# Optimization experiments

Measured on AMD Instinct MI355X. Metric: run time of the kernel, lower is better.

The kernel has to match this reference:

```python
import jax, jax.numpy as jnp
import numpy as np

B, S_IMG, S_TXT, H, D = 1, 2048, 512, 24, 128
HID = H * D  # 3072
S_TOT = S_TXT + S_IMG
IP_SCALE = 1.0
EPS = 1e-5


def setup_inputs() -> dict:
    key = jax.random.key(0)
    ks = jax.random.split(key, 16)
    r = lambda k, s: jax.random.normal(k, s, dtype=jnp.float32)
    w = lambda k, s: r(k, s) * 0.02
    theta = r(ks[15], (S_TOT, D))  # rotary angles over joint sequence
    z = lambda: jnp.zeros((HID,), jnp.float32)
    return dict(
        hidden_states=r(ks[0], (B, S_IMG, HID)),
        encoder_hidden_states=r(ks[1], (B, S_TXT, HID)),
        image_emb=r(ks[2], (B, 4, HID)),
        rope_cos=jnp.cos(theta), rope_sin=jnp.sin(theta),
        Wq=w(ks[3], (HID, HID)), bq=z(),
        Wk=w(ks[4], (HID, HID)), bk=z(),
        Wv=w(ks[5], (HID, HID)), bv=z(),
        Waq=w(ks[6], (HID, HID)), baq=z(),
        Wak=w(ks[7], (HID, HID)), bak=z(),
        Wav=w(ks[8], (HID, HID)), bav=z(),
        Wk_ip=w(ks[9], (HID, HID)),
        Wv_ip=w(ks[10], (HID, HID)),
        Wo=w(ks[11], (HID, HID)), bo=z(),
        Wao=w(ks[12], (HID, HID)), bao=z(),
    )


def _heads(x):  # [B,S,HID] -> [B,H,S,D]
    return x.reshape(x.shape[0], x.shape[1], H, D).transpose(0, 2, 1, 3)


def _unheads(x):  # [B,H,S,D] -> [B,S,HID]
    return x.transpose(0, 2, 1, 3).reshape(x.shape[0], x.shape[2], HID)


def _rmsnorm(x):  # over last dim, no affine (RMSNorm(128, affine=False))
    return x * jax.lax.rsqrt(jnp.mean(x * x, axis=-1, keepdims=True) + EPS)


def _rope(x, cos, sin):  # diffusers apply_rotary_emb, use_real, interleaved pairs
    xp = x.reshape(*x.shape[:-1], D // 2, 2)
    rot = jnp.stack([-xp[..., 1], xp[..., 0]], axis=-1).reshape(x.shape)
    return x * cos + rot * sin  # cos/sin [S,D] broadcast over [B,H,S,D]


def _sdpa(q, k, v):
    s = jnp.einsum('bhqd,bhkd->bhqk', q, k) / jnp.sqrt(jnp.asarray(D, q.dtype))
    return jnp.einsum('bhqk,bhkd->bhqd', jax.nn.softmax(s, axis=-1), v)


def _forward(hidden_states, encoder_hidden_states, image_emb, rope_cos, rope_sin,
             Wq, bq, Wk, bk, Wv, bv, Waq, baq, Wak, bak, Wav, bav,
             Wk_ip, Wv_ip, Wo, bo, Wao, bao):
    # main QKV over image-latent tokens
    q = _rmsnorm(_heads(hidden_states @ Wq.T + bq))
    k = _rmsnorm(_heads(hidden_states @ Wk.T + bk))
    v = _heads(hidden_states @ Wv.T + bv)
    # IP-adapter cross attention (query = latent q, kv from image_emb)
    k_ip = _rmsnorm(_heads(image_emb @ Wk_ip.T))
    v_ip = _heads(image_emb @ Wv_ip.T)
    ip_out = _unheads(_sdpa(q, k_ip, v_ip))  # [B,S_IMG,HID]
    # encoder (text) QKV, concat text-first as in Flux
    eq = _rmsnorm(_heads(encoder_hidden_states @ Waq.T + baq))
    ek = _rmsnorm(_heads(encoder_hidden_states @ Wak.T + bak))
    ev = _heads(encoder_hidden_states @ Wav.T + bav)
    q = jnp.concatenate([eq, q], axis=2)
    k = jnp.concatenate([ek, k], axis=2)
    v = jnp.concatenate([ev, v], axis=2)
    q = _rope(q, rope_cos, rope_sin)
    k = _rope(k, rope_cos, rope_sin)
    out = _unheads(_sdpa(q, k, v))  # [B,S_TOT,HID]
    enc_out, hid_out = out[:, :S_TXT], out[:, S_TXT:]
    hid_out = hid_out + IP_SCALE * ip_out
    hid_out = hid_out @ Wo.T + bo   # to_out[0] (+ identity dropout)
    enc_out = enc_out @ Wao.T + bao  # to_add_out
    return hid_out, enc_out


def reference(hidden_states, encoder_hidden_states, image_emb, rope_cos, rope_sin,
              Wq, bq, Wk, bk, Wv, bv, Waq, baq, Wak, bak, Wav, bav,
              Wk_ip, Wv_ip, Wo, bo, Wao, bao):
    return _forward(hidden_states, encoder_hidden_states, image_emb, rope_cos, rope_sin,
                    Wq, bq, Wk, bk, Wv, bv, Waq, baq, Wak, bak, Wav, bav,
                    Wk_ip, Wv_ip, Wo, bo, Wao, bao)
```

## Files before the change

### kernel.cpp

```cpp
#include <hip/hip_runtime.h>

typedef __bf16 bf16;
typedef __bf16 bf16x2 __attribute__((ext_vector_type(2)));
typedef __bf16 bf16x4 __attribute__((ext_vector_type(4)));
typedef __bf16 bf16x8 __attribute__((ext_vector_type(8)));
typedef float  f32x4  __attribute__((ext_vector_type(4)));

#define H_    24
#define D_    128
#define HID_  3072
#define SIMG_ 2048
#define STXT_ 512
#define STOT_ 2560
#define EPS_  1e-5f
#define SCALE_ 0.08838834764831845f
#define HH_   ((size_t)HID_*HID_)

typedef __attribute__((address_space(3))) unsigned int lds_uint;
typedef const __attribute__((address_space(1))) unsigned int glb_uint;
__device__ __forceinline__ void gll16(const void* g, void* l){
  __builtin_amdgcn_global_load_lds((glb_uint*)g, (lds_uint*)l, 16, 0, 0);
}

__device__ inline bf16x8 frag8f(const float* __restrict__ p){
  const f32x4 a = *(const f32x4*)p;
  const f32x4 b = *(const f32x4*)(p + 4);
  bf16x8 r;
  r[0]=(bf16)a[0]; r[1]=(bf16)a[1]; r[2]=(bf16)a[2]; r[3]=(bf16)a[3];
  r[4]=(bf16)b[0]; r[5]=(bf16)b[1]; r[6]=(bf16)b[2]; r[7]=(bf16)b[3];
  return r;
}

__device__ __forceinline__ void cvt8(const float* __restrict__ s, bf16* __restrict__ d, int i){
  const f32x4 a = *(const f32x4*)(s + i);
  const f32x4 b = *(const f32x4*)(s + i + 4);
  bf16x8 o;
  o[0]=(bf16)a[0]; o[1]=(bf16)a[1]; o[2]=(bf16)a[2]; o[3]=(bf16)a[3];
  o[4]=(bf16)b[0]; o[5]=(bf16)b[1]; o[6]=(bf16)b[2]; o[7]=(bf16)b[3];
  *(bf16x8*)(d + i) = o;
}

#define CONV_BLK 2048
__global__ __launch_bounds__(256) void k_prep(
    const float* __restrict__ HS, const float* __restrict__ ENC,
    const float* __restrict__ W0, const float* __restrict__ W1,
    const float* __restrict__ W2, const float* __restrict__ W3,
    const float* __restrict__ W4, const float* __restrict__ W5,
    const float* __restrict__ W6, const float* __restrict__ W7,
    const float* __restrict__ IMG,
    const float* __restrict__ Wkip, const float* __restrict__ Wvip,
    bf16* __restrict__ HSb, bf16* __restrict__ ENCb, bf16* __restrict__ Wb8,
    float* __restrict__ Kip, float* __restrict__ Vip)
{
  __shared__ float tile[4][128];
  const int bx = (int)blockIdx.x;
  const int t = (int)threadIdx.x;
  if (bx < 48){
    const bool isV = (bx >= 24);
    const int h = bx % 24;
    const float* Wm = isV ? Wvip : Wkip;
    const int w = t >> 6, l = t & 63;
    const int lr = l & 15, lg = l >> 4;
    const int col0 = h*128 + w*32;
    f32x4 acc0 = {}, acc1 = {};
    const float* arow = IMG + (size_t)((lr < 4) ? lr : 0)*HID_;
    const float* wr0 = Wm + (size_t)(col0 + lr)*HID_;
    const float* wr1 = Wm + (size_t)(col0 + 16 + lr)*HID_;
    for (int k0 = 0; k0 < HID_; k0 += 32){
      const bf16x8 af = frag8f(arow + k0 + lg*8);
      acc0 = __builtin_amdgcn_mfma_f32_16x16x32_bf16(af, frag8f(wr0 + k0 + lg*8), acc0, 0, 0, 0);
      acc1 = __builtin_amdgcn_mfma_f32_16x16x32_bf16(af, frag8f(wr1 + k0 + lg*8), acc1, 0, 0, 0);
    }
    if (lg == 0){
      #pragma unroll
      for (int r = 0; r < 4; r++){
        tile[r][w*32 + lr]      = acc0[r];
        tile[r][w*32 + 16 + lr] = acc1[r];
      }
    }
    __syncthreads();
    if (isV){
      const int e = t*2;
      const int j = e >> 7, d = e & 127;
      Vip[(size_t)(h*4 + j)*D_ + d]     = tile[j][d];
      Vip[(size_t)(h*4 + j)*D_ + d + 1] = tile[j][d + 1];
    } else {
      const float v0 = tile[w][2*l], v1 = tile[w][2*l + 1];
      float ss = v0*v0 + v1*v1;
      #pragma unroll
      for (int m = 1; m < 64; m <<= 1) ss += __shfl_xor(ss, m);
      const float rk = rsqrtf(ss*(1.0f/128.0f) + EPS_);
      Kip[(size_t)(h*4 + w)*D_ + 2*l]     = v0*rk;
      Kip[(size_t)(h*4 + w)*D_ + 2*l + 1] = v1*rk;
    }
  } else {
    for (int c = bx - 48; c < 20352; c += CONV_BLK){
      const float* s; bf16* d; int base;
      if (c < 1536){ s = HS;  d = HSb;  base = c*4096; }
      else if (c < 1920){ s = ENC; d = ENCb; base = (c - 1536)*4096; }
      else {
        const int idx = c - 1920;
        const int wi = idx / 2304;
        s = (wi==0)?W0:(wi==1)?W1:(wi==2)?W2:(wi==3)?W3:(wi==4)?W4:(wi==5)?W5:(wi==6)?W6:W7;
        d = Wb8 + (size_t)wi*HH_;
        base = (idx % 2304)*4096;
      }
      const int i = base + t*16;
      cvt8(s, d, i);
      cvt8(s, d, i + 8);
    }
  }
}

#define MFMA_ __builtin_amdgcn_mfma_f32_16x16x32_bf16
#define MM(bfr, n) \
    acc[0][n]=MFMA_(af0,bfr,acc[0][n],0,0,0); acc[1][n]=MFMA_(af1,bfr,acc[1][n],0,0,0); \
    acc[2][n]=MFMA_(af2,bfr,acc[2][n],0,0,0); acc[3][n]=MFMA_(af3,bfr,acc[3][n],0,0,0);
#define WAIT6  asm volatile("s_waitcnt vmcnt(6)" ::: "memory")
#define WAIT0  asm volatile("s_waitcnt vmcnt(0)" ::: "memory")
#define NOWAIT (void)0

__device__ __forceinline__ void gemm8_core(
    const bf16* __restrict__ A, const bf16* __restrict__ W,
    int mb, int nb,
    f32x4 (&acc)[4][4],
    bf16 (&Al)[3][128][64],
    bf16 (&Bl)[3][256][64])
{
  const int t = (int)threadIdx.x;
  const int w = t >> 6, l = t & 63;
  const int lr = l & 15, lg = l >> 4;
  const int wr = w >> 2, wc = w & 3;
  const int srow = t >> 3;
  const int soff = ((t & 7) ^ (srow & 7)) * 8;

  const bf16* Abase = A + (size_t)(mb + srow)*HID_ + soff;
  const bf16* Wbase = W + (size_t)(nb + srow)*HID_ + soff;

#define SA(buf, tt, i) gll16(Abase + (size_t)(i)*64*HID_ + (tt)*64, &Al[buf][0][0] + (i)*4096 + t*8)
#define SB(buf, tt, i) gll16(Wbase + (size_t)(i)*64*HID_ + (tt)*64, &Bl[buf][0][0] + (i)*4096 + t*8)

  const int arow_ = wr*64 + lr;
  const int brow_ = wc*64 + lr;
  const int sx = lr & 7;

  SA(0,0,0); SA(0,0,1); SB(0,0,0); SB(0,0,1); SB(0,0,2); SB(0,0,3);
  SA(1,1,0); SA(1,1,1); SB(1,1,0); SB(1,1,1); SB(1,1,2); SB(1,1,3);
  WAIT6;
  __builtin_amdgcn_s_barrier();

#define TILE(C, NXT, TT, PRE, TW)                                            \
  {                                                                          \
    const int s0_ = (lg^sx)*8, s1_ = ((4+lg)^sx)*8;                          \
    bf16x8 af0,af1,af2,af3,b0,b1;                                            \
    af0=*(const bf16x8*)&Al[C][arow_   ][s0_];                               \
    af1=*(const bf16x8*)&Al[C][arow_+16][s0_];                               \
    af2=*(const bf16x8*)&Al[C][arow_+32][s0_];                               \
    af3=*(const bf16x8*)&Al[C][arow_+48][s0_];                               \
    b0 =*(const bf16x8*)&Bl[C][brow_   ][s0_];                               \
    b1 =*(const bf16x8*)&Bl[C][brow_+16][s0_];                               \
    if (PRE){ SA(NXT,(TT)+2,0); SA(NXT,(TT)+2,1); }                          \
    __builtin_amdgcn_s_setprio(1); MM(b0,0) MM(b1,1)                         \
    __builtin_amdgcn_s_setprio(0);                                           \
    b0 =*(const bf16x8*)&Bl[C][brow_+32][s0_];                               \
    b1 =*(const bf16x8*)&Bl[C][brow_+48][s0_];                               \
    if (PRE){ SB(NXT,(TT)+2,0); SB(NXT,(TT)+2,1); }                          \
    __builtin_amdgcn_s_setprio(1); MM(b0,2) MM(b1,3)                         \
    __builtin_amdgcn_s_setprio(0);                                           \
    af0=*(const bf16x8*)&Al[C][arow_   ][s1_];                               \
    af1=*(const bf16x8*)&Al[C][arow_+16][s1_];                               \
    af2=*(const bf16x8*)&Al[C][arow_+32][s1_];                               \
    af3=*(const bf16x8*)&Al[C][arow_+48][s1_];                               \
    b0 =*(const bf16x8*)&Bl[C][brow_   ][s1_];                               \
    b1 =*(const bf16x8*)&Bl[C][brow_+16][s1_];                               \
    if (PRE){ SB(NXT,(TT)+2,2); SB(NXT,(TT)+2,3); }                          \
    __builtin_amdgcn_s_setprio(1); MM(b0,0) MM(b1,1)                         \
    __builtin_amdgcn_s_setprio(0);                                           \
    b0 =*(const bf16x8*)&Bl[C][brow_+32][s1_];                               \
    b1 =*(const bf16x8*)&Bl[C][brow_+48][s1_];                               \
    __builtin_amdgcn_s_setprio(1); MM(b0,2) MM(b1,3)                         \
    __builtin_amdgcn_s_setprio(0);                                           \
    TW;                                                                      \
    __builtin_amdgcn_s_barrier();                                            \
  }

  for (int base = 0; base < 45; base += 3){
    TILE(0, 2, base,   true, WAIT6);
    TILE(1, 0, base+1, true, WAIT6);
    TILE(2, 1, base+2, true, WAIT6);
  }
  TILE(0, 2, 45, true,  WAIT6);
  TILE(1, 0, 46, false, WAIT0);
  TILE(2, 1, 47, false, NOWAIT);
#undef TILE
#undef SA
#undef SB
}

__global__ __launch_bounds__(512, 1) void k_gemm8_qkv(
    const bf16* __restrict__ Ahid, const bf16* __restrict__ Aenc,
    const bf16* __restrict__ Wb,
    const float* bq, const float* bk, const float* bv,
    const float* baq, const float* bak, const float* bav,
    bf16* Cq, bf16* Ck, bf16* Cv, bf16* Ceq, bf16* Cek, bf16* Cev)
{
  __shared__ __align__(16) bf16 Al[3][128][64];
  __shared__ __align__(16) bf16 Bl[3][256][64];
  const int lin = (int)blockIdx.x;
  const int work = (lin & 7)*90 + (lin >> 3);
  const int mt = work / 36;
  const int ct = work % 36;
  const int which = ct % 3;
  const int nb = (ct/3)*256;
  const int enc = (mt >= 16) ? 1 : 0;
  const int mb = (enc ? (mt - 16) : mt)*128;
  const bf16* A = enc ? Aenc : Ahid;
  const int widx = which + enc*3;
  const bf16* W = Wb + (size_t)widx*HH_;
  const float* bias = (which==0) ? (enc?baq:bq) : (which==1) ? (enc?bak:bk) : (enc?bav:bv);
  bf16* Cm = (which==0) ? (enc?Ceq:Cq) : (which==1) ? (enc?Cek:Ck) : (enc?Cev:Cv);

  f32x4 acc[4][4] = {};
  gemm8_core(A, W, mb, nb, acc, Al, Bl);

  const int w = (int)(threadIdx.x >> 6), l = (int)(threadIdx.x & 63u);
  const int lr = l & 15, lg = l >> 4;
  const int wr = w >> 2, wc = w & 3;
  #pragma unroll
  for (int nf = 0; nf < 4; nf++){
    const int col = nb + wc*64 + nf*16 + lr;
    const float bvl = bias[col];
    #pragma unroll
    for (int m = 0; m < 4; m++){
      #pragma unroll
      for (int r = 0; r < 4; r++){
        const int row = mb + wr*64 + m*16 + lg*4 + r;
        Cm[(size_t)row*HID_ + col] = (bf16)(acc[m][nf][r] + bvl);
      }
    }
  }
}

__global__ __launch_bounds__(512, 1) void k_gemm8_out(
    const bf16* __restrict__ Ahid, const bf16* __restrict__ Aenc,
    const bf16* __restrict__ Wb,
    const float* bo, const float* bao, float* __restrict__ outp)
{
  __shared__ __align__(16) bf16 Al[3][128][64];
  __shared__ __align__(16) bf16 Bl[3][256][64];
  const int lin = (int)blockIdx.x;
  const int work = (lin & 7)*30 + (lin >> 3);
  const int mt = work / 12;
  const int nb = (work % 12)*256;
  const int enc = (mt >= 16) ? 1 : 0;
  const int mb = (enc ? (mt - 16) : mt)*128;
  const bf16* A = enc ? Aenc : Ahid;
  const bf16* W = Wb + (size_t)(enc ? 7 : 6)*HH_;
  const float* bias = enc ? bao : bo;
  float* C = outp + (enc ? (size_t)SIMG_*HID_ : 0);

  f32x4 acc[4][4] = {};
  gemm8_core(A, W, mb, nb, acc, Al, Bl);

  const int w = (int)(threadIdx.x >> 6), l = (int)(threadIdx.x & 63u);
  const int lr = l & 15, lg = l >> 4;
  const int wr = w >> 2, wc = w & 3;
  #pragma unroll
  for (int nf = 0; nf < 4; nf++){
    const int col = nb + wc*64 + nf*16 + lr;
    const float bvl = bias[col];
    #pragma unroll
    for (int m = 0; m < 4; m++){
      #pragma unroll
      for (int r = 0; r < 4; r++){
        const int row = mb + wr*64 + m*16 + lg*4 + r;
        C[(size_t)row*HID_ + col] = acc[m][nf][r] + bvl;
      }
    }
  }
}

__global__ __launch_bounds__(256) void k_finish_qk2(
    const bf16* __restrict__ rawQ, const bf16* __restrict__ rawK,
    const bf16* __restrict__ rawEQ, const bf16* __restrict__ rawEK,
    const float* __restrict__ cosT, const float* __restrict__ sinT,
    const float* __restrict__ Kip, const float* __restrict__ Vip,
    bf16* __restrict__ Qh, bf16* __restrict__ Kh, bf16* __restrict__ ipOut)
{
  const int wid = (int)blockIdx.x*4 + (int)(threadIdx.x >> 6);
  const int l = (int)(threadIdx.x & 63u);
  const int s = wid / H_;
  const int h = wid % H_;
  const bf16 *sq_, *sk_;
  if (s < STXT_){
    const size_t off = (size_t)s*HID_ + h*D_;
    sq_ = rawEQ + off; sk_ = rawEK + off;
  } else {
    const size_t off = (size_t)(s - STXT_)*HID_ + h*D_;
    sq_ = rawQ + off; sk_ = rawK + off;
  }
  const int d0 = 2*l, d1 = 2*l + 1;
  float q0 = sq_[d0], q1 = sq_[d1];
  float k0 = sk_[d0], k1 = sk_[d1];
  float ssq = q0*q0 + q1*q1;
  float ssk = k0*k0 + k1*k1;
  #pragma unroll
  for (int m = 1; m < 64; m <<= 1){ ssq += __shfl_xor(ssq, m); ssk += __shfl_xor(ssk, m); }
  const float rq = rsqrtf(ssq*(1.0f/128.0f) + EPS_);
  const float rk = rsqrtf(ssk*(1.0f/128.0f) + EPS_);
  q0 *= rq; q1 *= rq; k0 *= rk; k1 *= rk;
  const float c0 = cosT[(size_t)s*D_ + d0], c1 = cosT[(size_t)s*D_ + d1];
  const float s0 = sinT[(size_t)s*D_ + d0], s1 = sinT[(size_t)s*D_ + d1];
  const float qo0 = q0*c0 - q1*s0, qo1 = q1*c1 + q0*s1;
  const float ko0 = k0*c0 - k1*s0, ko1 = k1*c1 + k0*s1;
  const size_t qoff = ((size_t)h*STOT_ + s)*D_ + d0;
  Qh[qoff] = (bf16)qo0; Qh[qoff + 1] = (bf16)qo1;
  Kh[qoff] = (bf16)ko0; Kh[qoff + 1] = (bf16)ko1;

  if (s >= STXT_){
    const float* kb = Kip + (size_t)h*4*D_;
    const float* vb = Vip + (size_t)h*4*D_;
    float sc[4];
    #pragma unroll
    for (int j = 0; j < 4; j++) sc[j] = q0*kb[j*D_ + d0] + q1*kb[j*D_ + d1];
    #pragma unroll
    for (int m = 1; m < 64; m <<= 1){
      #pragma unroll
      for (int j = 0; j < 4; j++) sc[j] += __shfl_xor(sc[j], m);
    }
    const float mx = fmaxf(fmaxf(sc[0], sc[1]), fmaxf(sc[2], sc[3]));
    float p[4], ps = 0.f;
    #pragma unroll
    for (int j = 0; j < 4; j++){ p[j] = __expf((sc[j] - mx)*SCALE_); ps += p[j]; }
    const float inv = 1.0f/ps;
    float o0 = 0.f, o1 = 0.f;
    #pragma unroll
    for (int j = 0; j < 4; j++){ o0 += p[j]*vb[j*D_ + d0]; o1 += p[j]*vb[j*D_ + d1]; }
    const size_t dst = (size_t)(s - STXT_)*HID_ + h*D_;
    ipOut[dst + d0] = (bf16)(o0*inv);
    ipOut[dst + d1] = (bf16)(o1*inv);
  }
}

__global__ __launch_bounds__(256) void k_vtrans(
    const bf16* __restrict__ rawV, const bf16* __restrict__ rawEV,
    bf16* __restrict__ Vt)
{
  __shared__ bf16 lt[128*130];
  const int t = (int)threadIdx.x;
  const int stile = (int)blockIdx.x*128;
  const int h = (int)blockIdx.y;
  #pragma unroll
  for (int i = 0; i < 8; i++){
    const int sl = i*16 + (t >> 4);
    const int s = stile + sl;
    const bf16* src = (s < STXT_) ? (rawEV + (size_t)s*HID_) : (rawV + (size_t)(s - STXT_)*HID_);
    const bf16x8 v = *(const bf16x8*)(src + h*D_ + (t & 15)*8);
    #pragma unroll
    for (int j = 0; j < 8; j++) lt[((t & 15)*8 + j)*130 + sl] = v[j];
  }
  __syncthreads();
  #pragma unroll
  for (int j = 0; j < 4; j++){
    const int d = j*32 + (t >> 3);
    const int s0 = (t & 7)*16;
    bf16x8 a, b;
    #pragma unroll
    for (int k = 0; k < 4; k++){
      const bf16x2 p = *(const bf16x2*)(lt + d*130 + s0 + 2*k);
      a[2*k] = p[0]; a[2*k+1] = p[1];
    }
    #pragma unroll
    for (int k = 0; k < 4; k++){
      const bf16x2 p = *(const bf16x2*)(lt + d*130 + s0 + 8 + 2*k);
      b[2*k] = p[0]; b[2*k+1] = p[1];
    }
    bf16* dst = Vt + ((size_t)h*D_ + d)*STOT_ + stile + s0;
    *(bf16x8*)dst = a;
    *(bf16x8*)(dst + 8) = b;
  }
}

__global__ __launch_bounds__(256, 2) void k_flash3(
    const bf16* __restrict__ Q, const bf16* __restrict__ K,
    const bf16* __restrict__ Vt, const bf16* __restrict__ ipOut,
    bf16* __restrict__ attnOut)
{
  __shared__ __align__(16) bf16 Ks[2][64*128];
  __shared__ __align__(16) bf16 Vs[2][128*64];
  __shared__ __align__(16) bf16 plds[4][32*64];
  const int t = (int)threadIdx.x;
  const int w = t >> 6, l = t & 63;
  const int lr = l & 15, lg = l >> 4;
  const int lin = (int)blockIdx.x;
  const int work = (lin & 7)*60 + (lin >> 3);
  const int h = work / 20;
  const int qbase = (work % 20)*128 + w*32;
  const bf16* Qh = Q  + (size_t)h*STOT_*D_;
  const bf16* Kh = K  + (size_t)h*STOT_*D_;
  const bf16* Vh = Vt + (size_t)h*D_*STOT_;

  bf16x8 qf[2][4];
  #pragma unroll
  for (int qt = 0; qt < 2; qt++)
    #pragma unroll
    for (int kk = 0; kk < 4; kk++)
      qf[qt][kk] = *(const bf16x8*)(Qh + (size_t)(qbase + qt*16 + lr)*D_ + kk*32 + lg*8);

  f32x4 acc[2][8] = {};
  float mrun[2] = {-3.0e38f, -3.0e38f}, lrun[2] = {0.f, 0.f};

  const int krow = t >> 4, kslot = t & 15;
  const int vrow = t >> 3, vslot = t & 7;

  auto STAGE = [&](int buf, int kv){
    #pragma unroll
    for (int i = 0; i < 4; i++){
      const int r = i*16 + krow;
      gll16(Kh + (size_t)(kv + r)*D_ + ((kslot ^ (r & 7))*8),
            (void*)(&Ks[buf][0] + (size_t)t*8 + i*2048));
    }
    #pragma unroll
    for (int i = 0; i < 4; i++){
      const int r = i*32 + vrow;
      gll16(Vh + (size_t)r*STOT_ + kv + ((vslot ^ (r & 7))*8),
            (void*)(&Vs[buf][0] + (size_t)t*8 + i*2048));
    }
  };

  STAGE(0, 0);
  __syncthreads();
  int cur = 0;
  for (int kv = 0; kv < STOT_; kv += 64){
    if (kv + 64 < STOT_) STAGE(cur ^ 1, kv + 64);

    f32x4 st[2][4] = {};
    #pragma unroll
    for (int tt = 0; tt < 4; tt++){
      const int kr = tt*16 + lr;
      #pragma unroll
      for (int kk = 0; kk < 4; kk++){
        const bf16x8 kf = *(const bf16x8*)(&Ks[cur][0] + kr*128 + (((kk*4 + lg) ^ (kr & 7))*8));
        st[0][tt] = __builtin_amdgcn_mfma_f32_16x16x32_bf16(kf, qf[0][kk], st[0][tt], 0, 0, 0);
        st[1][tt] = __builtin_amdgcn_mfma_f32_16x16x32_bf16(kf, qf[1][kk], st[1][tt], 0, 0, 0);
      }
    }
    #pragma unroll
    for (int qt = 0; qt < 2; qt++){
      const int q = qt*16 + lr;
      float sv[4][4];
      float vmax = -3.0e38f;
      #pragma unroll
      for (int tt = 0; tt < 4; tt++)
        #pragma unroll
        for (int r = 0; r < 4; r++){ const float x = st[qt][tt][r]*SCALE_; sv[tt][r] = x; vmax = fmaxf(vmax, x); }
      vmax = fmaxf(vmax, __shfl_xor(vmax, 16));
      vmax = fmaxf(vmax, __shfl_xor(vmax, 32));
      const float mnew  = fmaxf(mrun[qt], vmax);
      const float alpha = __expf(mrun[qt] - mnew);
      float rs = 0.f;
      #pragma unroll
      for (int tt = 0; tt < 4; tt++){
        bf16x4 pq;
        #pragma unroll
        for (int r = 0; r < 4; r++){
          const float p = __expf(sv[tt][r] - mnew);
          rs += p;
          pq[r] = (bf16)p;
        }
        *(bf16x4*)(&plds[w][q*64 + (((tt*2 + (lg >> 1)) ^ (q & 7))*8) + (lg & 1)*4]) = pq;
      }
      rs += __shfl_xor(rs, 16);
      rs += __shfl_xor(rs, 32);
      lrun[qt] = lrun[qt]*alpha + rs;
      mrun[qt] = mnew;
      #pragma unroll
      for (int n = 0; n < 8; n++)
        #pragma unroll
        for (int r = 0; r < 4; r++) acc[qt][n][r] *= alpha;
    }
    #pragma unroll
    for (int ks = 0; ks < 2; ks++){
      const bf16x8 pb0 = *(const bf16x8*)(&plds[w][(lr)*64      + (((ks*4 + lg) ^ (lr & 7))*8)]);
      const bf16x8 pb1 = *(const bf16x8*)(&plds[w][(16 + lr)*64 + (((ks*4 + lg) ^ (lr & 7))*8)]);
      #pragma unroll
      for (int n = 0; n < 8; n++){
        const int vr = n*16 + lr;
        const bf16x8 vf = *(const bf16x8*)(&Vs[cur][0] + vr*64 + (((ks*4 + lg) ^ (vr & 7))*8));
        acc[0][n] = __builtin_amdgcn_mfma_f32_16x16x32_bf16(vf, pb0, acc[0][n], 0, 0, 0);
        acc[1][n] = __builtin_amdgcn_mfma_f32_16x16x32_bf16(vf, pb1, acc[1][n], 0, 0, 0);
      }
    }
    __syncthreads();
    cur ^= 1;
  }
  const bool hid = (qbase >= STXT_);
  #pragma unroll
  for (int qt = 0; qt < 2; qt++){
    const float inv = 1.0f/lrun[qt];
    const int row = qbase + qt*16 + lr;
    #pragma unroll
    for (int n = 0; n < 8; n++){
      const size_t cbase = (size_t)row*HID_ + h*D_ + n*16 + lg*4;
      if (hid){
        const bf16x4 ip = *(const bf16x4*)(ipOut + (size_t)(row - STXT_)*HID_ + h*D_ + n*16 + lg*4);
        bf16x4 o;
        #pragma unroll
        for (int r = 0; r < 4; r++) o[r] = (bf16)(acc[qt][n][r]*inv + (float)ip[r]);
        *(bf16x4*)(attnOut + cbase) = o;
      } else {
        bf16x4 o;
        #pragma unroll
        for (int r = 0; r < 4; r++) o[r] = (bf16)(acc[qt][n][r]*inv);
        *(bf16x4*)(attnOut + cbase) = o;
      }
    }
  }
}

extern "C" void kernel_launch(void* const* d_in, const int* in_sizes, int n_in,
                              void* d_out, int out_size, void* d_ws, size_t ws_size,
                              hipStream_t stream)
{
  const float* HS   = (const float*)d_in[0];
  const float* ENC  = (const float*)d_in[1];
  const float* IMG  = (const float*)d_in[2];
  const float* COS  = (const float*)d_in[3];
  const float* SIN  = (const float*)d_in[4];
  const float* Wq   = (const float*)d_in[5];  const float* bq  = (const float*)d_in[6];
  const float* Wk   = (const float*)d_in[7];  const float* bk  = (const float*)d_in[8];
  const float* Wv   = (const float*)d_in[9];  const float* bv  = (const float*)d_in[10];
  const float* Waq  = (const float*)d_in[11]; const float* baq = (const float*)d_in[12];
  const float* Wak  = (const float*)d_in[13]; const float* bak = (const float*)d_in[14];
  const float* Wav  = (const float*)d_in[15]; const float* bav = (const float*)d_in[16];
  const float* Wkip = (const float*)d_in[17]; const float* Wvip= (const float*)d_in[18];
  const float* Wo   = (const float*)d_in[19]; const float* bo  = (const float*)d_in[20];
  const float* Wao  = (const float*)d_in[21]; const float* bao = (const float*)d_in[22];

  char* wsb = (char*)d_ws;
  size_t off = 0;
  auto alloc = [&](size_t bytes) -> char* {
    char* p = wsb + off; off += (bytes + 255) & ~((size_t)255); return p;
  };
  bf16* rawQ   = (bf16*)alloc((size_t)SIMG_*HID_*2);
  bf16* rawK   = (bf16*)alloc((size_t)SIMG_*HID_*2);
  bf16* rawV   = (bf16*)alloc((size_t)SIMG_*HID_*2);
  bf16* rawEQ  = (bf16*)alloc((size_t)STXT_*HID_*2);
  bf16* rawEK  = (bf16*)alloc((size_t)STXT_*HID_*2);
  bf16* rawEV  = (bf16*)alloc((size_t)STXT_*HID_*2);
  bf16* Qb     = (bf16*)alloc((size_t)H_*STOT_*D_*2);
  bf16* Kb     = (bf16*)alloc((size_t)H_*STOT_*D_*2);
  bf16* Vtb    = (bf16*)alloc((size_t)H_*STOT_*D_*2);
  bf16* AOUT   = (bf16*)alloc((size_t)STOT_*HID_*2);
  bf16* IPOUT  = (bf16*)alloc((size_t)SIMG_*HID_*2);
  float* KIPF  = (float*)alloc((size_t)H_*4*D_*4);
  float* VIPF  = (float*)alloc((size_t)H_*4*D_*4);
  bf16* HSb    = (bf16*)alloc((size_t)SIMG_*HID_*2);
  bf16* ENCb   = (bf16*)alloc((size_t)STXT_*HID_*2);
  bf16* Wb8    = (bf16*)alloc((size_t)8*HH_*2);

  dim3 blk(256);
  dim3 blk512(512);
  k_prep<<<dim3(48 + CONV_BLK), blk, 0, stream>>>(HS, ENC, Wq, Wk, Wv, Waq, Wak, Wav, Wo, Wao,
                                                  IMG, Wkip, Wvip, HSb, ENCb, Wb8, KIPF, VIPF);
  k_gemm8_qkv<<<dim3(720), blk512, 0, stream>>>(HSb, ENCb, Wb8,
                                                bq, bk, bv, baq, bak, bav,
                                                rawQ, rawK, rawV, rawEQ, rawEK, rawEV);
  k_finish_qk2<<<dim3(15360), blk, 0, stream>>>(rawQ, rawK, rawEQ, rawEK, COS, SIN,
                                                KIPF, VIPF, Qb, Kb, IPOUT);
  k_vtrans<<<dim3(20,24), blk, 0, stream>>>(rawV, rawEV, Vtb);
  k_flash3<<<dim3(480), blk, 0, stream>>>(Qb, Kb, Vtb, IPOUT, AOUT);
  float* outp = (float*)d_out;
  k_gemm8_out<<<dim3(240), blk512, 0, stream>>>(AOUT + (size_t)STXT_*HID_, AOUT, Wb8, bo, bao, outp);
}
```

Baseline: 547.1 us.

## Restructure GEMM core to 4-wave blocks with 32-wide K tiles and two blocks per CU

Replaces the 8-wave 128x256 GEMM core (64-wide K slices, 48 iterations) with a 4-wave version that keeps the same 128x256 output tile but gives each wave a 64x128 sub-tile (32 accumulators). K is streamed in 32-wide slices over 96 iterations, using a new swizzled LDS layout that packs two rows per 64-element line. LDS per block halves, so launch bounds allow two blocks per CU, aiming for better latency hiding and fewer LDS reads per MFMA. In exchange, register pressure per wave doubles and barriers are twice as frequent.

```diff
diff --git a/kernel.cpp b/kernel.cpp
--- a/kernel.cpp
+++ b/kernel.cpp
@@ -113,99 +113,113 @@
 }
 
 #define MFMA_ __builtin_amdgcn_mfma_f32_16x16x32_bf16
-#define MM(bfr, n) \
-    acc[0][n]=MFMA_(af0,bfr,acc[0][n],0,0,0); acc[1][n]=MFMA_(af1,bfr,acc[1][n],0,0,0); \
-    acc[2][n]=MFMA_(af2,bfr,acc[2][n],0,0,0); acc[3][n]=MFMA_(af3,bfr,acc[3][n],0,0,0);
 #define WAIT6  asm volatile("s_waitcnt vmcnt(6)" ::: "memory")
 #define WAIT0  asm volatile("s_waitcnt vmcnt(0)" ::: "memory")
 #define NOWAIT (void)0
 
-__device__ __forceinline__ void gemm8_core(
+__device__ __forceinline__ void gemm4_core(
     const bf16* __restrict__ A, const bf16* __restrict__ W,
     int mb, int nb,
-    f32x4 (&acc)[4][4],
-    bf16 (&Al)[3][128][64],
-    bf16 (&Bl)[3][256][64])
+    f32x4 (&acc)[4][8],
+    bf16 (&Al)[3][4096],
+    bf16 (&Bl)[3][8192])
 {
   const int t = (int)threadIdx.x;
   const int w = t >> 6, l = t & 63;
   const int lr = l & 15, lg = l >> 4;
-  const int wr = w >> 2, wc = w & 3;
-  const int srow = t >> 3;
-  const int soff = ((t & 7) ^ (srow & 7)) * 8;
-
-  const bf16* Abase = A + (size_t)(mb + srow)*HID_ + soff;
-  const bf16* Wbase = W + (size_t)(nb + srow)*HID_ + soff;
-
-#define SA(buf, tt, i) gll16(Abase + (size_t)(i)*64*HID_ + (tt)*64, &Al[buf][0][0] + (i)*4096 + t*8)
-#define SB(buf, tt, i) gll16(Wbase + (size_t)(i)*64*HID_ + (tt)*64, &Bl[buf][0][0] + (i)*4096 + t*8)
-
-  const int arow_ = wr*64 + lr;
-  const int brow_ = wc*64 + lr;
-  const int sx = lr & 7;
-
-  SA(0,0,0); SA(0,0,1); SB(0,0,0); SB(0,0,1); SB(0,0,2); SB(0,0,3);
-  SA(1,1,0); SA(1,1,1); SB(1,1,0); SB(1,1,1); SB(1,1,2); SB(1,1,3);
-  WAIT6;
-  __builtin_amdgcn_s_barrier();
-
-#define TILE(C, NXT, TT, PRE, TW)                                            \
+  const int wr = w >> 1, wc = w & 1;
+
+  const int gdA0 = t,        gdA1 = 256 + t;
+  const int lA0 = gdA0 >> 3, lA1 = gdA1 >> 3;
+  const int gA0 = (gdA0 & 7) ^ (lA0 & 7), gA1 = (gdA1 & 7) ^ (lA1 & 7);
+  const bf16* Asrc0 = A + (size_t)(mb + 2*lA0 + (gA0 >> 2))*HID_ + (gA0 & 3)*8;
+  const bf16* Asrc1 = A + (size_t)(mb + 2*lA1 + (gA1 >> 2))*HID_ + (gA1 & 3)*8;
+  const int dA0 = gdA0*8, dA1 = gdA1*8;
+
+  const bf16* Bsrc0; const bf16* Bsrc1; const bf16* Bsrc2; const bf16* Bsrc3;
+  int dB0, dB1, dB2, dB3;
+  {
+    const int g0 = t, g1 = 256 + t, g2 = 512 + t, g3 = 768 + t;
+    const int l0 = g0>>3, l1 = g1>>3, l2 = g2>>3, l3 = g3>>3;
+    const int u0 = (g0&7)^(l0&7), u1 = (g1&7)^(l1&7), u2 = (g2&7)^(l2&7), u3 = (g3&7)^(l3&7);
+    Bsrc0 = W + (size_t)(nb + 2*l0 + (u0>>2))*HID_ + (u0&3)*8;
+    Bsrc1 = W + (size_t)(nb + 2*l1 + (u1>>2))*HID_ + (u1&3)*8;
+    Bsrc2 = W + (size_t)(nb + 2*l2 + (u2>>2))*HID_ + (u2&3)*8;
+    Bsrc3 = W + (size_t)(nb + 2*l3 + (u3>>2))*HID_ + (u3&3)*8;
+    dB0 = g0*8; dB1 = g1*8; dB2 = g2*8; dB3 = g3*8;
+  }
+
+#define SA4(buf, TT)  { gll16(Asrc0 + (TT)*32, &Al[buf][0] + dA0); \
+                        gll16(Asrc1 + (TT)*32, &Al[buf][0] + dA1); }
+#define SB4a(buf, TT) { gll16(Bsrc0 + (TT)*32, &Bl[buf][0] + dB0); \
+                        gll16(Bsrc1 + (TT)*32, &Bl[buf][0] + dB1); }
+#define SB4b(buf, TT) { gll16(Bsrc2 + (TT)*32, &Bl[buf][0] + dB2); \
+                        gll16(Bsrc3 + (TT)*32, &Bl[buf][0] + dB3); }
+
+  const int gx = ((((lr & 1) << 2) | lg) ^ ((lr >> 1) & 7)) * 8;
+  const int baseA = (wr*32 + (lr >> 1))*64 + gx;
+  const int baseB = (wc*64 + (lr >> 1))*64 + gx;
+
+#define MMN(bb, n) \
+    acc[0][n]=MFMA_(a0,bb,acc[0][n],0,0,0); acc[1][n]=MFMA_(a1,bb,acc[1][n],0,0,0); \
+    acc[2][n]=MFMA_(a2,bb,acc[2][n],0,0,0); acc[3][n]=MFMA_(a3,bb,acc[3][n],0,0,0);
+
+#define TILE4(C, NXT, TT, PRE, TW)                                           \
   {                                                                          \
-    const int s0_ = (lg^sx)*8, s1_ = ((4+lg)^sx)*8;                          \
-    bf16x8 af0,af1,af2,af3,b0,b1;                                            \
-    af0=*(const bf16x8*)&Al[C][arow_   ][s0_];                               \
-    af1=*(const bf16x8*)&Al[C][arow_+16][s0_];                               \
-    af2=*(const bf16x8*)&Al[C][arow_+32][s0_];                               \
-    af3=*(const bf16x8*)&Al[C][arow_+48][s0_];                               \
-    b0 =*(const bf16x8*)&Bl[C][brow_   ][s0_];                               \
-    b1 =*(const bf16x8*)&Bl[C][brow_+16][s0_];                               \
-    if (PRE){ SA(NXT,(TT)+2,0); SA(NXT,(TT)+2,1); }                          \
-    __builtin_amdgcn_s_setprio(1); MM(b0,0) MM(b1,1)                         \
+    bf16x8 a0,a1,a2,a3,b0,b1,b2,b3;                                          \
+    a0 = *(const bf16x8*)(&Al[C][0] + baseA);                                \
+    a1 = *(const bf16x8*)(&Al[C][0] + baseA + 512);                          \
+    a2 = *(const bf16x8*)(&Al[C][0] + baseA + 1024);                         \
+    a3 = *(const bf16x8*)(&Al[C][0] + baseA + 1536);                         \
+    b0 = *(const bf16x8*)(&Bl[C][0] + baseB);                                \
+    b1 = *(const bf16x8*)(&Bl[C][0] + baseB + 512);                          \
+    b2 = *(const bf16x8*)(&Bl[C][0] + baseB + 1024);                         \
+    b3 = *(const bf16x8*)(&Bl[C][0] + baseB + 1536);                         \
+    if (PRE){ SA4(NXT, (TT)+2); SB4a(NXT, (TT)+2); }                         \
+    __builtin_amdgcn_s_setprio(1);                                           \
+    MMN(b0,0) MMN(b1,1) MMN(b2,2) MMN(b3,3)                                  \
     __builtin_amdgcn_s_setprio(0);                                           \
-    b0 =*(const bf16x8*)&Bl[C][brow_+32][s0_];                               \
-    b1 =*(const bf16x8*)&Bl[C][brow_+48][s0_];                               \
-    if (PRE){ SB(NXT,(TT)+2,0); SB(NXT,(TT)+2,1); }                          \
-    __builtin_amdgcn_s_setprio(1); MM(b0,2) MM(b1,3)                         \
-    __builtin_amdgcn_s_setprio(0);                                           \
-    af0=*(const bf16x8*)&Al[C][arow_   ][s1_];                               \
-    af1=*(const bf16x8*)&Al[C][arow_+16][s1_];                               \
-    af2=*(const bf16x8*)&Al[C][arow_+32][s1_];                               \
-    af3=*(const bf16x8*)&Al[C][arow_+48][s1_];                               \
-    b0 =*(const bf16x8*)&Bl[C][brow_   ][s1_];                               \
-    b1 =*(const bf16x8*)&Bl[C][brow_+16][s1_];                               \
-    if (PRE){ SB(NXT,(TT)+2,2); SB(NXT,(TT)+2,3); }                          \
-    __builtin_amdgcn_s_setprio(1); MM(b0,0) MM(b1,1)                         \
-    __builtin_amdgcn_s_setprio(0);                                           \
-    b0 =*(const bf16x8*)&Bl[C][brow_+32][s1_];                               \
-    b1 =*(const bf16x8*)&Bl[C][brow_+48][s1_];                               \
-    __builtin_amdgcn_s_setprio(1); MM(b0,2) MM(b1,3)                         \
+    b0 = *(const bf16x8*)(&Bl[C][0] + baseB + 2048);                         \
+    b1 = *(const bf16x8*)(&Bl[C][0] + baseB + 2560);                         \
+    b2 = *(const bf16x8*)(&Bl[C][0] + baseB + 3072);                         \
+    b3 = *(const bf16x8*)(&Bl[C][0] + baseB + 3584);                         \
+    if (PRE){ SB4b(NXT, (TT)+2); }                                           \
+    __builtin_amdgcn_s_setprio(1);                                           \
+    MMN(b0,4) MMN(b1,5) MMN(b2,6) MMN(b3,7)                                  \
     __builtin_amdgcn_s_setprio(0);                                           \
     TW;                                                                      \
     __builtin_amdgcn_s_barrier();                                            \
   }
 
-  for (int base = 0; base < 45; base += 3){
-    TILE(0, 2, base,   true, WAIT6);
-    TILE(1, 0, base+1, true, WAIT6);
-    TILE(2, 1, base+2, true, WAIT6);
-  }
-  TILE(0, 2, 45, true,  WAIT6);
-  TILE(1, 0, 46, false, WAIT0);
-  TILE(2, 1, 47, false, NOWAIT);
-#undef TILE
-#undef SA
-#undef SB
-}
-
-__global__ __launch_bounds__(512, 1) void k_gemm8_qkv(
+  SA4(0,0); SB4a(0,0); SB4b(0,0);
+  SA4(1,1); SB4a(1,1); SB4b(1,1);
+  WAIT6;
+  __builtin_amdgcn_s_barrier();
+
+  for (int base = 0; base < 93; base += 3){
+    TILE4(0, 2, base,   true, WAIT6);
+    TILE4(1, 0, base+1, true, WAIT6);
+    TILE4(2, 1, base+2, true, WAIT6);
+  }
+  TILE4(0, 2, 93, true,  WAIT6);
+  TILE4(1, 0, 94, false, WAIT0);
+  TILE4(2, 1, 95, false, NOWAIT);
+#undef TILE4
+#undef MMN
+#undef SA4
+#undef SB4a
+#undef SB4b
+}
+
+__global__ __launch_bounds__(256, 2) void k_gemm4_qkv(
     const bf16* __restrict__ Ahid, const bf16* __restrict__ Aenc,
     const bf16* __restrict__ Wb,
     const float* bq, const float* bk, const float* bv,
     const float* baq, const float* bak, const float* bav,
     bf16* Cq, bf16* Ck, bf16* Cv, bf16* Ceq, bf16* Cek, bf16* Cev)
 {
-  __shared__ __align__(16) bf16 Al[3][128][64];
-  __shared__ __align__(16) bf16 Bl[3][256][64];
+  __shared__ __align__(16) bf16 Al[3][4096];
+  __shared__ __align__(16) bf16 Bl[3][8192];
   const int lin = (int)blockIdx.x;
   const int work = (lin & 7)*90 + (lin >> 3);
   const int mt = work / 36;
@@ -220,34 +234,34 @@
   const float* bias = (which==0) ? (enc?baq:bq) : (which==1) ? (enc?bak:bk) : (enc?bav:bv);
   bf16* Cm = (which==0) ? (enc?Ceq:Cq) : (which==1) ? (enc?Cek:Ck) : (enc?Cev:Cv);
 
-  f32x4 acc[4][4] = {};
-  gemm8_core(A, W, mb, nb, acc, Al, Bl);
+  f32x4 acc[4][8] = {};
+  gemm4_core(A, W, mb, nb, acc, Al, Bl);
 
   const int w = (int)(threadIdx.x >> 6), l = (int)(threadIdx.x & 63u);
   const int lr = l & 15, lg = l >> 4;
-  const int wr = w >> 2, wc = w & 3;
-  #pragma unroll
-  for (int nf = 0; nf < 4; nf++){
-    const int col = nb + wc*64 + nf*16 + lr;
+  const int wr = w >> 1, wc = w & 1;
+  #pragma unroll
+  for (int n = 0; n < 8; n++){
+    const int col = nb + wc*128 + n*16 + lr;
     const float bvl = bias[col];
     #pragma unroll
     for (int m = 0; m < 4; m++){
       #pragma unroll
       for (int r = 0; r < 4; r++){
         const int row = mb + wr*64 + m*16 + lg*4 + r;
-        Cm[(size_t)row*HID_ + col] = (bf16)(acc[m][nf][r] + bvl);
-      }
-    }
-  }
-}
-
-__global__ __launch_bounds__(512, 1) void k_gemm8_out(
+        Cm[(size_t)row*HID_ + col] = (bf16)(acc[m][n][r] + bvl);
+      }
+    }
+  }
+}
+
+__global__ __launch_bounds__(256, 2) void k_gemm4_out(
     const bf16* __restrict__ Ahid, const bf16* __restrict__ Aenc,
     const bf16* __restrict__ Wb,
     const float* bo, const float* bao, float* __restrict__ outp)
 {
-  __shared__ __align__(16) bf16 Al[3][128][64];
-  __shared__ __align__(16) bf16 Bl[3][256][64];
+  __shared__ __align__(16) bf16 Al[3][4096];
+  __shared__ __align__(16) bf16 Bl[3][8192];
   const int lin = (int)blockIdx.x;
   const int work = (lin & 7)*30 + (lin >> 3);
   const int mt = work / 12;
@@ -259,22 +273,22 @@
   const float* bias = enc ? bao : bo;
   float* C = outp + (enc ? (size_t)SIMG_*HID_ : 0);
 
-  f32x4 acc[4][4] = {};
-  gemm8_core(A, W, mb, nb, acc, Al, Bl);
+  f32x4 acc[4][8] = {};
+  gemm4_core(A, W, mb, nb, acc, Al, Bl);
 
   const int w = (int)(threadIdx.x >> 6), l = (int)(threadIdx.x & 63u);
   const int lr = l & 15, lg = l >> 4;
-  const int wr = w >> 2, wc = w & 3;
-  #pragma unroll
-  for (int nf = 0; nf < 4; nf++){
-    const int col = nb + wc*64 + nf*16 + lr;
+  const int wr = w >> 1, wc = w & 1;
+  #pragma unroll
+  for (int n = 0; n < 8; n++){
+    const int col = nb + wc*128 + n*16 + lr;
     const float bvl = bias[col];
     #pragma unroll
     for (int m = 0; m < 4; m++){
       #pragma unroll
       for (int r = 0; r < 4; r++){
         const int row = mb + wr*64 + m*16 + lg*4 + r;
-        C[(size_t)row*HID_ + col] = acc[m][nf][r] + bvl;
+        C[(size_t)row*HID_ + col] = acc[m][n][r] + bvl;
       }
     }
   }
@@ -560,16 +574,15 @@
   bf16* Wb8    = (bf16*)alloc((size_t)8*HH_*2);
 
   dim3 blk(256);
-  dim3 blk512(512);
   k_prep<<<dim3(48 + CONV_BLK), blk, 0, stream>>>(HS, ENC, Wq, Wk, Wv, Waq, Wak, Wav, Wo, Wao,
                                                   IMG, Wkip, Wvip, HSb, ENCb, Wb8, KIPF, VIPF);
-  k_gemm8_qkv<<<dim3(720), blk512, 0, stream>>>(HSb, ENCb, Wb8,
-                                                bq, bk, bv, baq, bak, bav,
-                                                rawQ, rawK, rawV, rawEQ, rawEK, rawEV);
+  k_gemm4_qkv<<<dim3(720), blk, 0, stream>>>(HSb, ENCb, Wb8,
+                                             bq, bk, bv, baq, bak, bav,
+                                             rawQ, rawK, rawV, rawEQ, rawEK, rawEV);
   k_finish_qk2<<<dim3(15360), blk, 0, stream>>>(rawQ, rawK, rawEQ, rawEK, COS, SIN,
                                                 KIPF, VIPF, Qb, Kb, IPOUT);
   k_vtrans<<<dim3(20,24), blk, 0, stream>>>(rawV, rawEV, Vtb);
   k_flash3<<<dim3(480), blk, 0, stream>>>(Qb, Kb, Vtb, IPOUT, AOUT);
   float* outp = (float*)d_out;
-  k_gemm8_out<<<dim3(240), blk512, 0, stream>>>(AOUT + (size_t)STXT_*HID_, AOUT, Wb8, bo, bao, outp);
-}
+  k_gemm4_out<<<dim3(240), blk, 0, stream>>>(AOUT + (size_t)STXT_*HID_, AOUT, Wb8, bo, bao, outp);
+}
```

Result: slower. 571.8 us (+4.5%).
